# Kernel optimization log

Hardware: AMD Instinct MI355X
Metric: run time of the kernel (lower is better)

## Reference

```python
import jax, jax.numpy as jnp
import numpy as np

K = 8          # circulant block size
H = 16         # heads


def circ_linear(x, w, b):
    """Block-circulant linear. x: [..., in], w: [p, q, K] (first column of each
    KxK circulant block), b: [p*K]. y[p] = sum_q circ(w[p,q]) @ x_block[q],
    computed as circular convolution via rFFT."""
    q = w.shape[1]
    xb = x.reshape(x.shape[:-1] + (q, K))            # [..., q, K]
    Fx = jnp.fft.rfft(xb, axis=-1)                    # [..., q, K//2+1]
    Fw = jnp.fft.rfft(w, axis=-1)                     # [p, q, K//2+1]
    Fy = jnp.einsum('pqf,...qf->...pf', Fw, Fx)
    y = jnp.fft.irfft(Fy, n=K, axis=-1)               # [..., p, K]
    return y.reshape(x.shape[:-1] + (-1,)) + b


def setup_inputs() -> dict:
    key = jax.random.key(0)
    ks = jax.random.split(key, 9)
    B, N, D = 2, 1024, 1024
    p = q = D // K
    std = 1.0 / np.sqrt(D)
    mk = lambda k: jax.random.normal(k, (p, q, K), dtype=jnp.float32) * std
    mb = lambda k: jax.random.normal(k, (D,), dtype=jnp.float32) * 0.01
    x = jax.random.normal(ks[0], (B, N, D), dtype=jnp.float32)
    # causal mask: True = masked out
    mask = (~jnp.tril(jnp.ones((N, N), dtype=bool)))[None, None]  # [1,1,N,N]
    return {
        'x': x, 'mask': mask,
        'wq': mk(ks[1]), 'bq': mb(ks[2]),
        'wk': mk(ks[3]), 'bk': mb(ks[4]),
        'wv': mk(ks[5]), 'bv': mb(ks[6]),
        'wo': mk(ks[7]), 'bo': mb(ks[8]),
    }


def reference(x, mask, wq, bq, wk, bk, wv, bv, wo, bo):
    B, N, D = x.shape
    dh = D // H
    heads = lambda a: a.reshape(B, N, H, dh).transpose(0, 2, 1, 3)  # [B,H,N,dh]
    qh = heads(circ_linear(x, wq, bq))
    kh = heads(circ_linear(x, wk, bk))
    vh = heads(circ_linear(x, wv, bv))
    attn = jnp.einsum('bhnd,bhmd->bhnm', qh, kh)
    attn = jnp.where(mask, -jnp.inf, attn)
    probs = jax.nn.softmax(attn / jnp.sqrt(jnp.float32(dh)), axis=-1)
    out = jnp.einsum('bhnm,bhmd->bhnd', probs, vh)
    out = out.transpose(0, 2, 1, 3).reshape(B, N, D)
    return circ_linear(out, wo, bo)
```

## Files before the change

### kernel.cpp

```cpp
#include <hip/hip_runtime.h>
#include <hip/hip_bf16.h>

#define DIM   1024
#define NSEQ  1024
#define BATCH 2
#define NHEAD 16
#define DH    64

typedef unsigned short u16;
typedef __attribute__((ext_vector_type(8))) short  short8;
typedef __attribute__((ext_vector_type(4))) float  f32x4;
typedef __attribute__((ext_vector_type(8))) unsigned short u16x8;
typedef __attribute__((ext_vector_type(4))) unsigned short u16x4;

#define EXP_SCALE 0.18033688011112042f
#define SLOT_BYTES 8704

__device__ __forceinline__ u16 f2bf(float f) {
  union { float f; unsigned u; } v; v.f = f;
  unsigned r = v.u + 0x7FFFu + ((v.u >> 16) & 1u);
  return (u16)(r >> 16);
}
__device__ __forceinline__ float bf2f(u16 u) {
  union { unsigned u; float f; } v; v.u = (unsigned)u << 16;
  return v.f;
}

#define GLD(src, dst)                                                          \
  __builtin_amdgcn_global_load_lds(                                           \
      (const __attribute__((address_space(1))) void*)(src),                   \
      (__attribute__((address_space(3))) void*)(dst), 16, 0, 0)

__global__ __launch_bounds__(256) void prep_bf16(
    const float* __restrict__ wq, const float* __restrict__ wk,
    const float* __restrict__ wv, const float* __restrict__ wo,
    const float* __restrict__ x,
    u16* __restrict__ Wd, u16* __restrict__ Xb) {
  const int bid = blockIdx.x;
  if (bid < 2048) {
    const int z = bid >> 9;
    const float* w = (z == 0) ? wq : (z == 1) ? wk : (z == 2) ? wv : wo;
    u16* out = Wd + (size_t)z * DIM * DIM;
    const int idx8 = (bid & 511) * 256 + threadIdx.x;
    const int r = idx8 >> 7;
    const int q = idx8 & 127;
    const int p = r >> 3, a = r & 7;
    const float* wrow = w + (size_t)(p * 128 + q) * 8;
    const float4 w0 = *(const float4*)(wrow);
    const float4 w1 = *(const float4*)(wrow + 4);
    const float wv8[8] = {w0.x, w0.y, w0.z, w0.w, w1.x, w1.y, w1.z, w1.w};
    u16x8 o;
#pragma unroll
    for (int j = 0; j < 8; ++j) o[j] = f2bf(wv8[(a - j) & 7]);
    ((u16x8*)out)[idx8] = o;
  } else {
    const int i = (bid - 2048) * 256 + threadIdx.x;
    const float4 a = ((const float4*)x)[2 * i];
    const float4 b = ((const float4*)x)[2 * i + 1];
    u16x8 o;
    o[0] = f2bf(a.x); o[1] = f2bf(a.y); o[2] = f2bf(a.z); o[3] = f2bf(a.w);
    o[4] = f2bf(b.x); o[5] = f2bf(b.y); o[6] = f2bf(b.z); o[7] = f2bf(b.w);
    ((u16x8*)Xb)[i] = o;
  }
}

__global__ __launch_bounds__(256, 2) void gemm_qkv(
    const u16* __restrict__ A, const u16* __restrict__ Wd,
    const float* __restrict__ bq, const float* __restrict__ bk,
    const float* __restrict__ bv,
    u16* __restrict__ Qb, u16* __restrict__ Kb, u16* __restrict__ Vt) {
  __shared__ u16 As[2][64 * 64];
  __shared__ u16 Bs[2][3 * 64 * 64];

  const int tid  = threadIdx.x;
  const int w    = tid >> 6, lane = tid & 63;
  const int nb   = blockIdx.x * 64;
  const int mb   = blockIdx.y * 64;

  f32x4 acc[3][2][2] = {};

  const int m0 = (w >> 1) * 32, n0 = (w & 1) * 32;
  const int lr = lane & 15, lg = lane >> 4;
  const int lsw = lr & 7;

#define STAGE(buf, k0)                                                         \
  do {                                                                         \
    _Pragma("unroll")                                                          \
    for (int i = 0; i < 2; ++i) {                                              \
      const int bc = i * 256 + w * 64;                                         \
      const int c  = bc + lane;                                                \
      const int row = c >> 3, js = (c & 7) ^ (row & 7);                        \
      GLD(A + (size_t)(mb + row) * DIM + (k0) + js * 8, As[buf] + bc * 8);     \
    }                                                                          \
    _Pragma("unroll")                                                          \
    for (int i = 0; i < 6; ++i) {                                              \
      const int bc = i * 256 + w * 64;                                         \
      const int c  = bc + lane;                                                \
      const int z  = c >> 9, ci = c & 511;                                     \
      const int row = ci >> 3, js = (ci & 7) ^ (row & 7);                      \
      GLD(Wd + (size_t)z * DIM * DIM + (size_t)(nb + row) * DIM + (k0) + js * 8,\
          Bs[buf] + bc * 8);                                                   \
    }                                                                          \
  } while (0)

  STAGE(0, 0);
  __syncthreads();
  int cur = 0;
  for (int k0 = 0; k0 < DIM; k0 += 64) {
    if (k0 + 64 < DIM) STAGE(cur ^ 1, k0 + 64);

#pragma unroll
    for (int kk = 0; kk < 2; ++kk) {
      const int sw = ((kk * 4 + lg) ^ lsw) * 8;
      short8 a[2], b[3][2];
#pragma unroll
      for (int mi = 0; mi < 2; ++mi)
        a[mi] = *(const short8*)&As[cur][(m0 + mi * 16 + lr) * 64 + sw];
#pragma unroll
      for (int z = 0; z < 3; ++z)
#pragma unroll
        for (int ni = 0; ni < 2; ++ni)
          b[z][ni] = *(const short8*)
              &Bs[cur][z * 4096 + (n0 + ni * 16 + lr) * 64 + sw];
#pragma unroll
      for (int z = 0; z < 3; ++z)
#pragma unroll
        for (int mi = 0; mi < 2; ++mi)
#pragma unroll
          for (int ni = 0; ni < 2; ++ni)
            acc[z][mi][ni] = __builtin_amdgcn_mfma_f32_16x16x32_bf16(
                a[mi], b[z][ni], acc[z][mi][ni], 0, 0, 0);
    }

    __syncthreads();
    cur ^= 1;
  }
#undef STAGE

  const int col = lane & 15, rq4 = (lane >> 4) * 4;

#pragma unroll
  for (int z = 0; z < 2; ++z) {
    u16* C = z ? Kb : Qb;
    const float* bias = z ? bk : bq;
#pragma unroll
    for (int ni = 0; ni < 2; ++ni) {
      const int gc = nb + n0 + ni * 16 + col;
      const float bb = bias[gc];
#pragma unroll
      for (int mi = 0; mi < 2; ++mi) {
        const size_t rbase = (size_t)(mb + m0 + mi * 16 + rq4) * DIM + gc;
#pragma unroll
        for (int j = 0; j < 4; ++j)
          C[rbase + (size_t)j * DIM] = f2bf(acc[z][mi][ni][j] + bb);
      }
    }
  }
  {
    const int b = mb >> 10;
    const int h = blockIdx.x;
    const int nbase = (mb & (NSEQ - 1)) + m0;
#pragma unroll
    for (int ni = 0; ni < 2; ++ni) {
      const int dh = n0 + ni * 16 + col;
      const float bb = bv[nb + dh];
      u16* vrow = Vt + ((size_t)(b * NHEAD + h) * DH + dh) * NSEQ;
#pragma unroll
      for (int mi = 0; mi < 2; ++mi) {
        const int nn = nbase + mi * 16 + rq4;
        u16x4 o;
#pragma unroll
        for (int j = 0; j < 4; ++j) o[j] = f2bf(acc[2][mi][ni][j] + bb);
        *(u16x4*)(vrow + nn) = o;
      }
    }
  }
}

__global__ __launch_bounds__(256, 2) void gemm_o(
    const u16* __restrict__ A, const u16* __restrict__ W,
    const float* __restrict__ bias, float* __restrict__ C) {
  __shared__ u16 As[2][64 * 64];
  __shared__ u16 Bs[2][64 * 64];

  const int tid  = threadIdx.x;
  const int w    = tid >> 6, lane = tid & 63;
  const int mb   = blockIdx.y * 64, nb = blockIdx.x * 64;

  f32x4 acc[2][2] = {};

  const int m0 = (w >> 1) * 32, n0 = (w & 1) * 32;
  const int lr = lane & 15, lg = lane >> 4;
  const int lsw = lr & 7;

#define STAGE(buf, k0)                                                         \
  do {                                                                         \
    _Pragma("unroll")                                                          \
    for (int i = 0; i < 2; ++i) {                                              \
      const int bc = i * 256 + w * 64;                                         \
      const int c  = bc + lane;                                                \
      const int row = c >> 3, js = (c & 7) ^ (row & 7);                        \
      GLD(A + (size_t)(mb + row) * DIM + (k0) + js * 8, As[buf] + bc * 8);     \
      GLD(W + (size_t)(nb + row) * DIM + (k0) + js * 8, Bs[buf] + bc * 8);     \
    }                                                                          \
  } while (0)

  STAGE(0, 0);
  __syncthreads();
  int cur = 0;
  for (int k0 = 0; k0 < DIM; k0 += 64) {
    if (k0 + 64 < DIM) STAGE(cur ^ 1, k0 + 64);

#pragma unroll
    for (int kk = 0; kk < 2; ++kk) {
      const int sw = ((kk * 4 + lg) ^ lsw) * 8;
      short8 a[2], b[2];
#pragma unroll
      for (int mi = 0; mi < 2; ++mi)
        a[mi] = *(const short8*)&As[cur][(m0 + mi * 16 + lr) * 64 + sw];
#pragma unroll
      for (int ni = 0; ni < 2; ++ni)
        b[ni] = *(const short8*)&Bs[cur][(n0 + ni * 16 + lr) * 64 + sw];
#pragma unroll
      for (int mi = 0; mi < 2; ++mi)
#pragma unroll
        for (int ni = 0; ni < 2; ++ni)
          acc[mi][ni] = __builtin_amdgcn_mfma_f32_16x16x32_bf16(
              a[mi], b[ni], acc[mi][ni], 0, 0, 0);
    }

    __syncthreads();
    cur ^= 1;
  }
#undef STAGE

  const int col = lane & 15, rq = (lane >> 4) * 4;
#pragma unroll
  for (int ni = 0; ni < 2; ++ni) {
    const int gc = nb + n0 + ni * 16 + col;
    const float bv = bias[gc];
#pragma unroll
    for (int mi = 0; mi < 2; ++mi) {
      const size_t rbase = (size_t)(mb + m0 + mi * 16 + rq) * DIM + gc;
#pragma unroll
      for (int j = 0; j < 4; ++j)
        C[rbase + (size_t)j * DIM] = acc[mi][ni][j] + bv;
    }
  }
}

__global__ __launch_bounds__(256, 3) void attn_split(
    const u16* __restrict__ Qg, const u16* __restrict__ Kg,
    const u16* __restrict__ Vt, char* __restrict__ Part,
    u16* __restrict__ AOb) {
  const int bid = blockIdx.x;
  const int s   = bid >> 3;
  const int g   = (bid & 7) * 4 + s / 51;
  const int b   = g >> 4, h = g & 15;
  int idx = s % 51, qt = 0, cc = 0;
  for (int t = 15; t >= 0; --t) {
    const int nc = t / 3 + 1;
    if (idx < nc) { qt = t; cc = idx; break; }
    idx -= nc;
  }
  const int tid = threadIdx.x;
  const int w  = tid >> 6, l = tid & 63;
  const int lr = l & 15, lg = l >> 4;

  __shared__ u16 Klds[3][64 * 64];
  __shared__ u16 Vlds[3][64 * 64];

  const int qg = qt * 64 + w * 16 + lr;
  const size_t base_bh = (size_t)b * NSEQ * DIM + (size_t)h * DH;
  const size_t vt_bh   = (size_t)(b * NHEAD + h) * DH * NSEQ;

  short8 qf[2];
#pragma unroll
  for (int c = 0; c < 2; ++c)
    qf[c] = *(const short8*)(Qg + base_bh + (size_t)qg * DIM + c * 32 + lg * 8);

  f32x4 acc_o[4] = {};
  float m_run = -1e30f, l_run = 0.f;

  const int srow8 = l >> 3;
  const int sj    = l & 7;

  const int kt0 = cc * 3;
  const int nt  = min(kt0 + 3, qt + 1) - kt0;

#pragma unroll
  for (int t = 0; t < 3; ++t) {
    if (t < nt) {
      const int kt = kt0 + t;
#pragma unroll
      for (int i = 0; i < 2; ++i) {
        const int cb  = w * 2 + i;
        const int row = cb * 8 + srow8;
        const int c16 = sj ^ (row & 7);
        GLD(Kg + base_bh + (size_t)(kt * 64 + row) * DIM + c16 * 8,
            Klds[t] + cb * 512);
        GLD(Vt + vt_bh + (size_t)row * NSEQ + kt * 64 + c16 * 8,
            Vlds[t] + cb * 512);
      }
    }
  }
  __syncthreads();

  for (int it = 0; it < nt; ++it) {
    const int kt = kt0 + it;

    f32x4 s4[4] = {};
#pragma unroll
    for (int t16 = 0; t16 < 4; ++t16) {
      const int row = t16 * 16 + lr;
#pragma unroll
      for (int c = 0; c < 2; ++c) {
        const int c16 = (c * 4 + lg) ^ (row & 7);
        const short8 kf = *(const short8*)
            ((const char*)Klds[it] + row * 128 + c16 * 16);
        s4[t16] = __builtin_amdgcn_mfma_f32_16x16x32_bf16(kf, qf[c], s4[t16], 0, 0, 0);
      }
    }

    const bool diag = (kt == qt);
    float mloc = -1e30f;
#pragma unroll
    for (int t16 = 0; t16 < 4; ++t16)
#pragma unroll
      for (int j = 0; j < 4; ++j) {
        float v = s4[t16][j];
        if (diag && (kt * 64 + t16 * 16 + lg * 4 + j) > qg) v = -1e30f;
        s4[t16][j] = v;
        mloc = fmaxf(mloc, v);
      }
    mloc = fmaxf(mloc, __shfl_xor(mloc, 16));
    mloc = fmaxf(mloc, __shfl_xor(mloc, 32));
    const float m_new = fmaxf(m_run, mloc);
    const float a = exp2f((m_run - m_new) * EXP_SCALE);
    float psum = 0.f;
#pragma unroll
    for (int t16 = 0; t16 < 4; ++t16)
#pragma unroll
      for (int j = 0; j < 4; ++j) {
        const float p = exp2f((s4[t16][j] - m_new) * EXP_SCALE);
        psum += p;
        s4[t16][j] = p;
      }
    psum += __shfl_xor(psum, 16);
    psum += __shfl_xor(psum, 32);
    l_run = l_run * a + psum;
    m_run = m_new;
#pragma unroll
    for (int d = 0; d < 4; ++d) acc_o[d] *= a;

#pragma unroll
    for (int c = 0; c < 2; ++c) {
      unsigned a0, a1, b0, b1;
      asm("v_cvt_pk_bf16_f32 %0, %1, %2"
          : "=v"(a0) : "v"(s4[2 * c][0]), "v"(s4[2 * c][1]));
      asm("v_cvt_pk_bf16_f32 %0, %1, %2"
          : "=v"(a1) : "v"(s4[2 * c][2]), "v"(s4[2 * c][3]));
      asm("v_cvt_pk_bf16_f32 %0, %1, %2"
          : "=v"(b0) : "v"(s4[2 * c + 1][0]), "v"(s4[2 * c + 1][1]));
      asm("v_cvt_pk_bf16_f32 %0, %1, %2"
          : "=v"(b1) : "v"(s4[2 * c + 1][2]), "v"(s4[2 * c + 1][3]));
      asm("v_permlane32_swap_b32 %0, %1" : "+v"(a0), "+v"(b0));
      asm("v_permlane16_swap_b32 %0, %1" : "+v"(a0), "+v"(b0));
      asm("v_permlane32_swap_b32 %0, %1" : "+v"(a1), "+v"(b1));
      asm("v_permlane16_swap_b32 %0, %1" : "+v"(a1), "+v"(b1));
      union { unsigned u[4]; short8 s; } pu;
      pu.u[0] = a0; pu.u[1] = a1; pu.u[2] = b0; pu.u[3] = b1;
      const short8 pf = pu.s;
#pragma unroll
      for (int d = 0; d < 4; ++d) {
        const int dh = d * 16 + lr;
        const int c16 = (c * 4 + lg) ^ (dh & 7);
        const short8 vf = *(const short8*)
            ((const char*)Vlds[it] + dh * 128 + c16 * 16);
        acc_o[d] = __builtin_amdgcn_mfma_f32_16x16x32_bf16(vf, pf, acc_o[d], 0, 0, 0);
      }
    }
  }

  const int ql = w * 16 + lr;
  if (qt < 3) {
    const float inv = 1.f / l_run;
    u16* Op = AOb + (size_t)(b * NSEQ + qt * 64 + ql) * DIM + (size_t)h * DH;
#pragma unroll
    for (int d = 0; d < 4; ++d) {
      u16x4 o;
      o[0] = f2bf(acc_o[d][0] * inv); o[1] = f2bf(acc_o[d][1] * inv);
      o[2] = f2bf(acc_o[d][2] * inv); o[3] = f2bf(acc_o[d][3] * inv);
      *(u16x4*)(Op + d * 16 + lg * 4) = o;
    }
  } else {
    char* slot = Part +
        (size_t)(((b * NHEAD + h) * 16 + qt) * 6 + cc) * SLOT_BYTES;
    u16* Po = (u16*)slot;
    float* Pm = (float*)(slot + 8192);
#pragma unroll
    for (int d = 0; d < 4; ++d) {
      u16x4 o;
      o[0] = f2bf(acc_o[d][0]); o[1] = f2bf(acc_o[d][1]);
      o[2] = f2bf(acc_o[d][2]); o[3] = f2bf(acc_o[d][3]);
      *(u16x4*)(Po + ql * 64 + d * 16 + lg * 4) = o;
    }
    if (lg == 0) {
      Pm[ql]      = m_run;
      Pm[64 + ql] = l_run;
    }
  }
}

__global__ __launch_bounds__(256) void attn_merge(
    const char* __restrict__ Part, u16* __restrict__ AOb) {
  const int bid = blockIdx.x;
  const int x   = bid & 7;
  const int i   = bid >> 3;
  const int g   = x * 4 + i / 13;
  const int b   = g >> 4, h = g & 15;
  const int qt  = i % 13 + 3;
  const int t = threadIdx.x;
  const int q = t >> 2, quad = t & 3;
  const int nc = qt / 3 + 1;
  const char* base = Part +
      (size_t)(((b * NHEAD + h) * 16 + qt) * 6) * SLOT_BYTES;

  float mv[6], lv[6], fc[6];
  float M = -1e30f;
  for (int c = 0; c < nc; ++c) {
    const float* Pm = (const float*)(base + (size_t)c * SLOT_BYTES + 8192);
    mv[c] = Pm[q];
    lv[c] = Pm[64 + q];
    M = fmaxf(M, mv[c]);
  }
  float L = 0.f;
  for (int c = 0; c < nc; ++c) {
    fc[c] = exp2f((mv[c] - M) * EXP_SCALE);
    L += lv[c] * fc[c];
  }
  const float inv = 1.f / L;

  float o[16] = {};
  for (int c = 0; c < nc; ++c) {
    const u16* Po = (const u16*)(base + (size_t)c * SLOT_BYTES) +
                    q * 64 + quad * 16;
    const float f = fc[c];
    const u16x8 v0 = *(const u16x8*)(Po);
    const u16x8 v1 = *(const u16x8*)(Po + 8);
#pragma unroll
    for (int j = 0; j < 8; ++j) {
      o[j]     += f * bf2f(v0[j]);
      o[8 + j] += f * bf2f(v1[j]);
    }
  }

  u16* dst = AOb + (size_t)(b * NSEQ + qt * 64 + q) * DIM + h * DH + quad * 16;
  u16x8 o0, o1;
#pragma unroll
  for (int j = 0; j < 8; ++j) { o0[j] = f2bf(o[j] * inv); o1[j] = f2bf(o[8 + j] * inv); }
  *(u16x8*)(dst)     = o0;
  *(u16x8*)(dst + 8) = o1;
}

extern "C" void kernel_launch(void* const* d_in, const int* in_sizes, int n_in,
                              void* d_out, int out_size, void* d_ws, size_t ws_size,
                              hipStream_t stream) {
  const float* x  = (const float*)d_in[0];
  const float* wq = (const float*)d_in[2];
  const float* bq = (const float*)d_in[3];
  const float* wk = (const float*)d_in[4];
  const float* bk = (const float*)d_in[5];
  const float* wv = (const float*)d_in[6];
  const float* bv = (const float*)d_in[7];
  const float* wo = (const float*)d_in[8];
  const float* bo = (const float*)d_in[9];

  char* ws = (char*)d_ws;
  u16* Wd    = (u16*)(ws);
  u16* Xb    = (u16*)(ws + ((size_t)8  << 20));
  u16* Qb    = (u16*)(ws + ((size_t)12 << 20));
  u16* Kb    = (u16*)(ws + ((size_t)16 << 20));
  u16* Vt    = (u16*)(ws + ((size_t)24 << 20));
  u16* AOb   = (u16*)(ws + ((size_t)28 << 20));
  char* Prt  = (char*)(ws + ((size_t)32 << 20));

  prep_bf16<<<dim3(3072, 1, 1), 256, 0, stream>>>(wq, wk, wv, wo, x, Wd, Xb);

  gemm_qkv<<<dim3(NHEAD, (BATCH * NSEQ) / 64, 1), 256, 0, stream>>>(
      Xb, Wd, bq, bk, bv, Qb, Kb, Vt);

  attn_split<<<dim3(1632, 1, 1), 256, 0, stream>>>(Qb, Kb, Vt, Prt, AOb);

  attn_merge<<<dim3(416, 1, 1), 256, 0, stream>>>(Prt, AOb);

  gemm_o<<<dim3(DIM / 64, (BATCH * NSEQ) / 64, 1), 256, 0, stream>>>(
      AOb, Wd + (size_t)3 * DIM * DIM, bo, (float*)d_out);
}
```

Baseline: 70.32 us.

## Process two 64-row query tiles per attention block to reuse K/V tiles

Each split-attention block now handles 128 query rows (two 64-row groups) against the same staged K/V tiles in LDS, so every K/V load is used for twice as many queries. The block count roughly halves and the partial-result slots and merge kernel are re-indexed for 128-row query tiles. In exchange, register pressure rises from the doubled accumulators and Q fragments, which may hurt occupancy at launch bounds of 3. There are also fewer blocks to spread across CUs.

```diff
diff --git a/kernel.cpp b/kernel.cpp
--- a/kernel.cpp
+++ b/kernel.cpp
@@ -14,7 +14,7 @@
 typedef __attribute__((ext_vector_type(4))) unsigned short u16x4;
 
 #define EXP_SCALE 0.18033688011112042f
-#define SLOT_BYTES 8704
+#define SLOT2_BYTES 17408
 
 __device__ __forceinline__ u16 f2bf(float f) {
   union { float f; unsigned u; } v; v.f = f;
@@ -255,11 +255,11 @@
     u16* __restrict__ AOb) {
   const int bid = blockIdx.x;
   const int s   = bid >> 3;
-  const int g   = (bid & 7) * 4 + s / 51;
+  const int g   = (bid & 7) * 4 + s / 27;
   const int b   = g >> 4, h = g & 15;
-  int idx = s % 51, qt = 0, cc = 0;
-  for (int t = 15; t >= 0; --t) {
-    const int nc = t / 3 + 1;
+  int idx = s % 27, qt = 0, cc = 0;
+  for (int t = 7; t >= 0; --t) {
+    const int nc = (2 * t + 4) / 3;
     if (idx < nc) { qt = t; cc = idx; break; }
     idx -= nc;
   }
@@ -270,23 +270,26 @@
   __shared__ u16 Klds[3][64 * 64];
   __shared__ u16 Vlds[3][64 * 64];
 
-  const int qg = qt * 64 + w * 16 + lr;
   const size_t base_bh = (size_t)b * NSEQ * DIM + (size_t)h * DH;
   const size_t vt_bh   = (size_t)(b * NHEAD + h) * DH * NSEQ;
 
-  short8 qf[2];
-#pragma unroll
-  for (int c = 0; c < 2; ++c)
-    qf[c] = *(const short8*)(Qg + base_bh + (size_t)qg * DIM + c * 32 + lg * 8);
-
-  f32x4 acc_o[4] = {};
-  float m_run = -1e30f, l_run = 0.f;
+  short8 qf[2][2];
+#pragma unroll
+  for (int g2 = 0; g2 < 2; ++g2)
+#pragma unroll
+    for (int c = 0; c < 2; ++c)
+      qf[g2][c] = *(const short8*)
+          (Qg + base_bh +
+           (size_t)(qt * 128 + g2 * 64 + w * 16 + lr) * DIM + c * 32 + lg * 8);
+
+  f32x4 acc_o[2][4] = {};
+  float m_run[2] = {-1e30f, -1e30f}, l_run[2] = {0.f, 0.f};
 
   const int srow8 = l >> 3;
   const int sj    = l & 7;
 
   const int kt0 = cc * 3;
-  const int nt  = min(kt0 + 3, qt + 1) - kt0;
+  const int nt  = min(kt0 + 3, 2 * qt + 2) - kt0;
 
 #pragma unroll
   for (int t = 0; t < 3; ++t) {
@@ -309,105 +312,120 @@
   for (int it = 0; it < nt; ++it) {
     const int kt = kt0 + it;
 
-    f32x4 s4[4] = {};
-#pragma unroll
-    for (int t16 = 0; t16 < 4; ++t16) {
-      const int row = t16 * 16 + lr;
+#pragma unroll
+    for (int g2 = 0; g2 < 2; ++g2) {
+      if (kt > 2 * qt + g2) continue;
+
+      f32x4 s4[4] = {};
+#pragma unroll
+      for (int t16 = 0; t16 < 4; ++t16) {
+        const int row = t16 * 16 + lr;
+#pragma unroll
+        for (int c = 0; c < 2; ++c) {
+          const int c16 = (c * 4 + lg) ^ (row & 7);
+          const short8 kf = *(const short8*)
+              ((const char*)Klds[it] + row * 128 + c16 * 16);
+          s4[t16] = __builtin_amdgcn_mfma_f32_16x16x32_bf16(
+              kf, qf[g2][c], s4[t16], 0, 0, 0);
+        }
+      }
+
+      const bool diag = (kt == 2 * qt + g2);
+      const int qgrow = qt * 128 + g2 * 64 + w * 16 + lr;
+      float mloc = -1e30f;
+#pragma unroll
+      for (int t16 = 0; t16 < 4; ++t16)
+#pragma unroll
+        for (int j = 0; j < 4; ++j) {
+          float v = s4[t16][j];
+          if (diag && (kt * 64 + t16 * 16 + lg * 4 + j) > qgrow) v = -1e30f;
+          s4[t16][j] = v;
+          mloc = fmaxf(mloc, v);
+        }
+      mloc = fmaxf(mloc, __shfl_xor(mloc, 16));
+      mloc = fmaxf(mloc, __shfl_xor(mloc, 32));
+      const float m_new = fmaxf(m_run[g2], mloc);
+      const float a = exp2f((m_run[g2] - m_new) * EXP_SCALE);
+      float psum = 0.f;
+#pragma unroll
+      for (int t16 = 0; t16 < 4; ++t16)
+#pragma unroll
+        for (int j = 0; j < 4; ++j) {
+          const float p = exp2f((s4[t16][j] - m_new) * EXP_SCALE);
+          psum += p;
+          s4[t16][j] = p;
+        }
+      psum += __shfl_xor(psum, 16);
+      psum += __shfl_xor(psum, 32);
+      l_run[g2] = l_run[g2] * a + psum;
+      m_run[g2] = m_new;
+#pragma unroll
+      for (int d = 0; d < 4; ++d) acc_o[g2][d] *= a;
+
 #pragma unroll
       for (int c = 0; c < 2; ++c) {
-        const int c16 = (c * 4 + lg) ^ (row & 7);
-        const short8 kf = *(const short8*)
-            ((const char*)Klds[it] + row * 128 + c16 * 16);
-        s4[t16] = __builtin_amdgcn_mfma_f32_16x16x32_bf16(kf, qf[c], s4[t16], 0, 0, 0);
-      }
-    }
-
-    const bool diag = (kt == qt);
-    float mloc = -1e30f;
-#pragma unroll
-    for (int t16 = 0; t16 < 4; ++t16)
-#pragma unroll
-      for (int j = 0; j < 4; ++j) {
-        float v = s4[t16][j];
-        if (diag && (kt * 64 + t16 * 16 + lg * 4 + j) > qg) v = -1e30f;
-        s4[t16][j] = v;
-        mloc = fmaxf(mloc, v);
-      }
-    mloc = fmaxf(mloc, __shfl_xor(mloc, 16));
-    mloc = fmaxf(mloc, __shfl_xor(mloc, 32));
-    const float m_new = fmaxf(m_run, mloc);
-    const float a = exp2f((m_run - m_new) * EXP_SCALE);
-    float psum = 0.f;
-#pragma unroll
-    for (int t16 = 0; t16 < 4; ++t16)
-#pragma unroll
-      for (int j = 0; j < 4; ++j) {
-        const float p = exp2f((s4[t16][j] - m_new) * EXP_SCALE);
-        psum += p;
-        s4[t16][j] = p;
-      }
-    psum += __shfl_xor(psum, 16);
-    psum += __shfl_xor(psum, 32);
-    l_run = l_run * a + psum;
-    m_run = m_new;
-#pragma unroll
-    for (int d = 0; d < 4; ++d) acc_o[d] *= a;
-
-#pragma unroll
-    for (int c = 0; c < 2; ++c) {
-      unsigned a0, a1, b0, b1;
-      asm("v_cvt_pk_bf16_f32 %0, %1, %2"
-          : "=v"(a0) : "v"(s4[2 * c][0]), "v"(s4[2 * c][1]));
-      asm("v_cvt_pk_bf16_f32 %0, %1, %2"
-          : "=v"(a1) : "v"(s4[2 * c][2]), "v"(s4[2 * c][3]));
-      asm("v_cvt_pk_bf16_f32 %0, %1, %2"
-          : "=v"(b0) : "v"(s4[2 * c + 1][0]), "v"(s4[2 * c + 1][1]));
-      asm("v_cvt_pk_bf16_f32 %0, %1, %2"
-          : "=v"(b1) : "v"(s4[2 * c + 1][2]), "v"(s4[2 * c + 1][3]));
-      asm("v_permlane32_swap_b32 %0, %1" : "+v"(a0), "+v"(b0));
-      asm("v_permlane16_swap_b32 %0, %1" : "+v"(a0), "+v"(b0));
-      asm("v_permlane32_swap_b32 %0, %1" : "+v"(a1), "+v"(b1));
-      asm("v_permlane16_swap_b32 %0, %1" : "+v"(a1), "+v"(b1));
-      union { unsigned u[4]; short8 s; } pu;
-      pu.u[0] = a0; pu.u[1] = a1; pu.u[2] = b0; pu.u[3] = b1;
-      const short8 pf = pu.s;
+        unsigned a0, a1, b0, b1;
+        asm("v_cvt_pk_bf16_f32 %0, %1, %2"
+            : "=v"(a0) : "v"(s4[2 * c][0]), "v"(s4[2 * c][1]));
+        asm("v_cvt_pk_bf16_f32 %0, %1, %2"
+            : "=v"(a1) : "v"(s4[2 * c][2]), "v"(s4[2 * c][3]));
+        asm("v_cvt_pk_bf16_f32 %0, %1, %2"
+            : "=v"(b0) : "v"(s4[2 * c + 1][0]), "v"(s4[2 * c + 1][1]));
+        asm("v_cvt_pk_bf16_f32 %0, %1, %2"
+            : "=v"(b1) : "v"(s4[2 * c + 1][2]), "v"(s4[2 * c + 1][3]));
+        asm("v_permlane32_swap_b32 %0, %1" : "+v"(a0), "+v"(b0));
+        asm("v_permlane16_swap_b32 %0, %1" : "+v"(a0), "+v"(b0));
+        asm("v_permlane32_swap_b32 %0, %1" : "+v"(a1), "+v"(b1));
+        asm("v_permlane16_swap_b32 %0, %1" : "+v"(a1), "+v"(b1));
+        union { unsigned u[4]; short8 s; } pu;
+        pu.u[0] = a0; pu.u[1] = a1; pu.u[2] = b0; pu.u[3] = b1;
+        const short8 pf = pu.s;
+#pragma unroll
+        for (int d = 0; d < 4; ++d) {
+          const int dh = d * 16 + lr;
+          const int c16 = (c * 4 + lg) ^ (dh & 7);
+          const short8 vf = *(const short8*)
+              ((const char*)Vlds[it] + dh * 128 + c16 * 16);
+          acc_o[g2][d] = __builtin_amdgcn_mfma_f32_16x16x32_bf16(
+              vf, pf, acc_o[g2][d], 0, 0, 0);
+        }
+      }
+    }
+  }
+
+  const int ql = w * 16 + lr;
+  if (qt == 0) {
+#pragma unroll
+    for (int g2 = 0; g2 < 2; ++g2) {
+      const float inv = 1.f / l_run[g2];
+      u16* Op = AOb + (size_t)(b * NSEQ + g2 * 64 + ql) * DIM + (size_t)h * DH;
 #pragma unroll
       for (int d = 0; d < 4; ++d) {
-        const int dh = d * 16 + lr;
-        const int c16 = (c * 4 + lg) ^ (dh & 7);
-        const short8 vf = *(const short8*)
-            ((const char*)Vlds[it] + dh * 128 + c16 * 16);
-        acc_o[d] = __builtin_amdgcn_mfma_f32_16x16x32_bf16(vf, pf, acc_o[d], 0, 0, 0);
-      }
-    }
-  }
-
-  const int ql = w * 16 + lr;
-  if (qt < 3) {
-    const float inv = 1.f / l_run;
-    u16* Op = AOb + (size_t)(b * NSEQ + qt * 64 + ql) * DIM + (size_t)h * DH;
-#pragma unroll
-    for (int d = 0; d < 4; ++d) {
-      u16x4 o;
-      o[0] = f2bf(acc_o[d][0] * inv); o[1] = f2bf(acc_o[d][1] * inv);
-      o[2] = f2bf(acc_o[d][2] * inv); o[3] = f2bf(acc_o[d][3] * inv);
-      *(u16x4*)(Op + d * 16 + lg * 4) = o;
+        u16x4 o;
+        o[0] = f2bf(acc_o[g2][d][0] * inv); o[1] = f2bf(acc_o[g2][d][1] * inv);
+        o[2] = f2bf(acc_o[g2][d][2] * inv); o[3] = f2bf(acc_o[g2][d][3] * inv);
+        *(u16x4*)(Op + d * 16 + lg * 4) = o;
+      }
     }
   } else {
     char* slot = Part +
-        (size_t)(((b * NHEAD + h) * 16 + qt) * 6 + cc) * SLOT_BYTES;
+        (size_t)(((b * NHEAD + h) * 8 + qt) * 6 + cc) * SLOT2_BYTES;
     u16* Po = (u16*)slot;
-    float* Pm = (float*)(slot + 8192);
-#pragma unroll
-    for (int d = 0; d < 4; ++d) {
-      u16x4 o;
-      o[0] = f2bf(acc_o[d][0]); o[1] = f2bf(acc_o[d][1]);
-      o[2] = f2bf(acc_o[d][2]); o[3] = f2bf(acc_o[d][3]);
-      *(u16x4*)(Po + ql * 64 + d * 16 + lg * 4) = o;
-    }
-    if (lg == 0) {
-      Pm[ql]      = m_run;
-      Pm[64 + ql] = l_run;
+    float* Pm = (float*)(slot + 16384);
+#pragma unroll
+    for (int g2 = 0; g2 < 2; ++g2) {
+      const int row = g2 * 64 + ql;
+#pragma unroll
+      for (int d = 0; d < 4; ++d) {
+        u16x4 o;
+        o[0] = f2bf(acc_o[g2][d][0]); o[1] = f2bf(acc_o[g2][d][1]);
+        o[2] = f2bf(acc_o[g2][d][2]); o[3] = f2bf(acc_o[g2][d][3]);
+        *(u16x4*)(Po + row * 64 + d * 16 + lg * 4) = o;
+      }
+      if (lg == 0) {
+        Pm[row]       = m_run[g2];
+        Pm[128 + row] = l_run[g2];
+      }
     }
   }
 }
@@ -417,21 +435,24 @@
   const int bid = blockIdx.x;
   const int x   = bid & 7;
   const int i   = bid >> 3;
-  const int g   = x * 4 + i / 13;
+  const int g   = x * 4 + i / 14;
   const int b   = g >> 4, h = g & 15;
-  const int qt  = i % 13 + 3;
+  const int rem = i % 14;
+  const int qt  = rem / 2 + 1;
+  const int hh  = rem & 1;
   const int t = threadIdx.x;
   const int q = t >> 2, quad = t & 3;
-  const int nc = qt / 3 + 1;
+  const int row = hh * 64 + q;
+  const int nc = (2 * qt + 4) / 3;
   const char* base = Part +
-      (size_t)(((b * NHEAD + h) * 16 + qt) * 6) * SLOT_BYTES;
+      (size_t)(((b * NHEAD + h) * 8 + qt) * 6) * SLOT2_BYTES;
 
   float mv[6], lv[6], fc[6];
   float M = -1e30f;
   for (int c = 0; c < nc; ++c) {
-    const float* Pm = (const float*)(base + (size_t)c * SLOT_BYTES + 8192);
-    mv[c] = Pm[q];
-    lv[c] = Pm[64 + q];
+    const float* Pm = (const float*)(base + (size_t)c * SLOT2_BYTES + 16384);
+    mv[c] = Pm[row];
+    lv[c] = Pm[128 + row];
     M = fmaxf(M, mv[c]);
   }
   float L = 0.f;
@@ -443,8 +464,8 @@
 
   float o[16] = {};
   for (int c = 0; c < nc; ++c) {
-    const u16* Po = (const u16*)(base + (size_t)c * SLOT_BYTES) +
-                    q * 64 + quad * 16;
+    const u16* Po = (const u16*)(base + (size_t)c * SLOT2_BYTES) +
+                    row * 64 + quad * 16;
     const float f = fc[c];
     const u16x8 v0 = *(const u16x8*)(Po);
     const u16x8 v1 = *(const u16x8*)(Po + 8);
@@ -455,7 +476,7 @@
     }
   }
 
-  u16* dst = AOb + (size_t)(b * NSEQ + qt * 64 + q) * DIM + h * DH + quad * 16;
+  u16* dst = AOb + (size_t)(b * NSEQ + qt * 128 + row) * DIM + h * DH + quad * 16;
   u16x8 o0, o1;
 #pragma unroll
   for (int j = 0; j < 8; ++j) { o0[j] = f2bf(o[j] * inv); o1[j] = f2bf(o[8 + j] * inv); }
@@ -490,9 +511,9 @@
   gemm_qkv<<<dim3(NHEAD, (BATCH * NSEQ) / 64, 1), 256, 0, stream>>>(
       Xb, Wd, bq, bk, bv, Qb, Kb, Vt);
 
-  attn_split<<<dim3(1632, 1, 1), 256, 0, stream>>>(Qb, Kb, Vt, Prt, AOb);
-
-  attn_merge<<<dim3(416, 1, 1), 256, 0, stream>>>(Prt, AOb);
+  attn_split<<<dim3(864, 1, 1), 256, 0, stream>>>(Qb, Kb, Vt, Prt, AOb);
+
+  attn_merge<<<dim3(448, 1, 1), 256, 0, stream>>>(Prt, AOb);
 
   gemm_o<<<dim3(DIM / 64, (BATCH * NSEQ) / 64, 1), 256, 0, stream>>>(
       AOb, Wd + (size_t)3 * DIM * DIM, bo, (float*)d_out);
```

New measurement: 72.38 us. +2.9%, slower.
